# Performance work log

Measured on AMD Instinct MI355X. Metric: run time of the kernel, lower is better.

Reference implementation:

```python
import jax, jax.numpy as jnp
import numpy as np

N_E = 50000
N_R = 1000
E = 800000
E_HIDDEN = 256
R_HIDDEN = 64
NEG_SLOPE = 0.01  # torch F.leaky_relu default


def segment_softmax(logits, seg, num_segments):
    # numerically stable per-segment softmax over edges
    seg_max = jax.ops.segment_max(logits, seg, num_segments=num_segments)
    seg_max = jnp.where(jnp.isfinite(seg_max), seg_max, 0.0)
    ex = jnp.exp(logits - seg_max[seg])
    denom = jax.ops.segment_sum(ex, seg, num_segments=num_segments)
    return ex / (denom[seg] + 1e-16)


def setup_inputs() -> dict:
    key = jax.random.key(0)
    ks = jax.random.split(key, 9)
    return {
        "x_e": jax.random.normal(ks[0], (N_E, E_HIDDEN), dtype=jnp.float32),
        "x_r": jax.random.normal(ks[1], (N_R, R_HIDDEN), dtype=jnp.float32),
        "edge_index": jax.random.randint(ks[2], (2, E), 0, N_E, dtype=jnp.int64),
        "rel": jax.random.randint(ks[3], (E,), 0, N_R, dtype=jnp.int64),
        "line_graph_index": jax.random.randint(ks[4], (2, E), 0, E, dtype=jnp.int64),
        "line_graph_val": jax.random.uniform(ks[5], (E,), dtype=jnp.float32),
        "a_h_w": jax.random.normal(ks[6], (E_HIDDEN,), dtype=jnp.float32),
        "a_t_w": jax.random.normal(ks[7], (E_HIDDEN,), dtype=jnp.float32),
        "a_r_w": jax.random.normal(ks[8], (R_HIDDEN,), dtype=jnp.float32),
    }


def reference(x_e, x_r, edge_index, rel, line_graph_index, line_graph_val, a_h_w, a_t_w, a_r_w):
    head, tail = edge_index[0], edge_index[1]
    # per-node scalar scores, gathered per edge
    s_e_h = jnp.einsum("nd,d->n", x_e, a_h_w)  # [N_e]
    s_e_t = jnp.einsum("nd,d->n", x_e, a_t_w)  # [N_e]
    s_r = jnp.einsum("rd,d->r", x_r, a_r_w)    # [N_r]
    e_h = s_e_h[head]
    e_t = s_e_t[tail]
    e_r = s_r[rel]

    n_e = x_e.shape[0]
    msg = x_r[rel]  # [E, r_hidden]

    # head branch: segment softmax over head groups, scatter-aggregate x_r[rel]
    alpha_h = segment_softmax(jax.nn.leaky_relu(e_h + e_r, NEG_SLOPE), head, n_e)
    x_e_h = jax.ops.segment_sum(alpha_h[:, None] * msg, head, num_segments=n_e)

    # tail branch: softmax grouped by tail, but spmm still scatters into head rows
    alpha_t = segment_softmax(jax.nn.leaky_relu(e_t + e_r, NEG_SLOPE), tail, n_e)
    x_e_t = jax.ops.segment_sum(alpha_t[:, None] * msg, tail, num_segments=n_e)

    return jnp.concatenate([x_e_h, x_e_t], axis=1)  # [N_e, 2*r_hidden]
```

## Files before the change

### kernel.cpp

```cpp
#include <hip/hip_runtime.h>

static constexpr int kNE = 50000;
static constexpr int kNR = 1000;
static constexpr int kE  = 800000;
static constexpr int kEH = 256;
static constexpr int kRH = 64;
static constexpr float kNeg = 0.01f;

static constexpr int kSegsPerB = 64;
static constexpr int kSegs = 2 * kNE;
static constexpr int kB = (kSegs + kSegsPerB - 1) / kSegsPerB;
static constexpr int kCap = 1536;
static constexpr int kEdgesPerBin = 2048;
static constexpr int kChunkRecs  = 2 * kEdgesPerBin;
static constexpr int kBinBlocks  = (kE + kEdgesPerBin - 1) / kEdgesPerBin;
static constexpr int kTabW       = kB + 1;
static constexpr int kNodeBlocks = kNE / 8;
static constexpr int kRelBlocks  = kNR / 8;
static constexpr int kCntPad = 2048;

__device__ __forceinline__ float lrelu(float x){ return x > 0.f ? x : kNeg * x; }

__global__ __launch_bounds__(512) void k_bin_scores(
        const float* __restrict__ xe, const float* __restrict__ ahw,
        const float* __restrict__ atw, const float* __restrict__ xr,
        const float* __restrict__ arw,
        const int* __restrict__ head, const int* __restrict__ tail,
        const int* __restrict__ rel,
        float* __restrict__ s_h, float* __restrict__ s_t, float* __restrict__ s_r,
        unsigned short* __restrict__ chunk, unsigned short* __restrict__ tab){
    __shared__ int cnt[kCntPad];
    __shared__ int cur[kCntPad];
    __shared__ unsigned int srt[kChunkRecs];
    __shared__ int wsum[8];

    int blk = blockIdx.x;
    int tid = threadIdx.x;
    int lane = tid & 63;

    if (blk >= kBinBlocks){
        int sb = blk - kBinBlocks;
        if (sb < kNodeBlocks){
            int node = sb * 8 + (tid >> 6);
            const float4* row = (const float4*)(xe + (size_t)node * kEH);
            float4 xv = row[lane];
            float4 av = ((const float4*)ahw)[lane];
            float4 bv = ((const float4*)atw)[lane];
            float ph = xv.x*av.x + xv.y*av.y + xv.z*av.z + xv.w*av.w;
            float pt = xv.x*bv.x + xv.y*bv.y + xv.z*bv.z + xv.w*bv.w;
            #pragma unroll
            for (int o = 32; o > 0; o >>= 1){
                ph += __shfl_down(ph, o, 64);
                pt += __shfl_down(pt, o, 64);
            }
            if (lane == 0){ s_h[node] = ph; s_t[node] = pt; }
        } else {
            int r = (sb - kNodeBlocks) * 8 + (tid >> 6);
            float p = xr[(size_t)r * kRH + lane] * arw[lane];
            #pragma unroll
            for (int o = 32; o > 0; o >>= 1) p += __shfl_down(p, o, 64);
            if (lane == 0) s_r[r] = p;
        }
        return;
    }

    int e0 = blk * kEdgesPerBin;
    for (int i = tid; i < kCntPad; i += 512) cnt[i] = 0;
    __syncthreads();

    unsigned int recs[8];
    unsigned short rnk[8];
    #pragma unroll
    for (int p = 0; p < 4; ++p){
        int e = e0 + p * 512 + tid;
        unsigned int rh = 0xFFFFFFFFu, rt = 0xFFFFFFFFu;
        unsigned short kh = 0, kt = 0;
        if (e < kE){
            int h = head[e], t = tail[e], r = rel[e];
            rh = ((unsigned int)h << 10) | (unsigned int)r;
            rt = ((unsigned int)(kNE + t) << 10) | (unsigned int)r;
            kh = (unsigned short)atomicAdd(&cnt[rh >> 16], 1);
            kt = (unsigned short)atomicAdd(&cnt[rt >> 16], 1);
        }
        recs[p] = rh; recs[4 + p] = rt;
        rnk[p]  = kh; rnk[4 + p]  = kt;
    }
    __syncthreads();

    int c0 = cnt[4 * tid], c1 = cnt[4 * tid + 1], c2 = cnt[4 * tid + 2], c3 = cnt[4 * tid + 3];
    int v = c0 + c1 + c2 + c3;
    int x = v;
    #pragma unroll
    for (int o = 1; o < 64; o <<= 1){
        int y = __shfl_up(x, o, 64);
        if (lane >= o) x += y;
    }
    int wv = tid >> 6;
    if (lane == 63) wsum[wv] = x;
    __syncthreads();
    int wpre = 0, tot = 0;
    #pragma unroll
    for (int w = 0; w < 8; ++w){
        int s = wsum[w];
        if (w < wv) wpre += s;
        tot += s;
    }
    int base = wpre + x - v;
    cur[4 * tid]     = base;
    cur[4 * tid + 1] = base + c0;
    cur[4 * tid + 2] = base + c0 + c1;
    cur[4 * tid + 3] = base + c0 + c1 + c2;
    __syncthreads();

    #pragma unroll
    for (int p = 0; p < 8; ++p){
        unsigned int rc = recs[p];
        if (rc != 0xFFFFFFFFu){
            int slot = cur[rc >> 16] + (int)rnk[p];
            srt[slot] = rc;
        }
    }
    __syncthreads();

    unsigned int* cw = (unsigned int*)(chunk + (size_t)blk * kChunkRecs);
    for (int j2 = tid; j2 < (tot >> 1); j2 += 512){
        unsigned int lo = srt[2 * j2] & 0xFFFFu;
        unsigned int hi = srt[2 * j2 + 1] & 0xFFFFu;
        cw[j2] = lo | (hi << 16);
    }
    unsigned short* trow = tab + (size_t)blk * kTabW;
    for (int i = tid; i < kB; i += 512) trow[i] = (unsigned short)cur[i];
    if (tid == 0) trow[kB] = (unsigned short)tot;
}

__global__ __launch_bounds__(256) void k_sort_aggregate(
        const unsigned short* __restrict__ chunk, const unsigned short* __restrict__ tab,
        const float* __restrict__ s_h, const float* __restrict__ s_t,
        const float* __restrict__ s_r, const float* __restrict__ xr,
        float* __restrict__ out){
    __shared__ float srl[kNR];
    __shared__ float sn[kSegsPerB];
    __shared__ unsigned short relbuf[kCap];
    __shared__ float alphabuf[kCap];
    __shared__ int cumOff[kBinBlocks + 1];
    __shared__ int srcBase[kBinBlocks];
    __shared__ int cnt[kSegsPerB], start[kSegsPerB];
    __shared__ unsigned int mx[kSegsPerB];
    __shared__ unsigned short order[kSegsPerB];
    __shared__ int gsum[4];

    int b = blockIdx.x;
    int tid = threadIdx.x;
    int lane = tid & 63;
    int wv = tid >> 6;

    for (int i = tid; i < kNR; i += 256) srl[i] = s_r[i];
    if (tid < kSegsPerB){
        cnt[tid] = 0;
        mx[tid] = 0u;
        int gseg = b * kSegsPerB + tid;
        float s = 0.f;
        if (gseg < kNE) s = s_h[gseg];
        else if (gseg < kSegs) s = s_t[gseg - kNE];
        sn[tid] = s;
    }
    if (tid == 0) cumOff[0] = 0;
    __syncthreads();

    int nrecBase = 0;
    for (int c0 = 0; c0 < kBinBlocks; c0 += 256){
        int c = c0 + tid;
        int L = 0;
        if (c < kBinBlocks){
            const unsigned short* trow = tab + (size_t)c * kTabW;
            int s = trow[b];
            L = (int)trow[b + 1] - s;
            srcBase[c] = c * kChunkRecs + s;
        }
        int x = L;
        #pragma unroll
        for (int o = 1; o < 64; o <<= 1){
            int y = __shfl_up(x, o, 64);
            if (lane >= o) x += y;
        }
        if (lane == 63) gsum[wv] = x;
        __syncthreads();
        int wpre = 0, stot = 0;
        #pragma unroll
        for (int w = 0; w < 4; ++w){
            int g = gsum[w];
            if (w < wv) wpre += g;
            stot += g;
        }
        if (c < kBinBlocks) cumOff[c + 1] = nrecBase + wpre + x;
        nrecBase += stot;
        __syncthreads();
    }
    int nrec = nrecBase > kCap ? kCap : nrecBase;

    unsigned short recs[6], rnk[6];
    #pragma unroll
    for (int p = 0; p < 6; ++p){
        int j = p * 256 + tid;
        unsigned short rc = 0xFFFFu, rk = 0;
        if (j < nrec){
            int lo = 0, hi = kBinBlocks;
            #pragma unroll 1
            while (hi - lo > 1){
                int mid = (lo + hi) >> 1;
                if (cumOff[mid] <= j) lo = mid; else hi = mid;
            }
            rc = chunk[srcBase[lo] + (j - cumOff[lo])];
            rk = (unsigned short)atomicAdd(&cnt[rc >> 10], 1);
        }
        recs[p] = rc; rnk[p] = rk;
    }
    __syncthreads();
    if (tid < kSegsPerB){
        int c = cnt[tid];
        int x = c;
        #pragma unroll
        for (int o = 1; o < 64; o <<= 1){
            int y = __shfl_up(x, o, 64);
            if (tid >= o) x += y;
        }
        start[tid] = x - c;

        unsigned int key = ((unsigned int)c << 6) | (unsigned int)tid;
        #pragma unroll
        for (int k = 2; k <= 64; k <<= 1){
            #pragma unroll
            for (int j = k >> 1; j > 0; j >>= 1){
                unsigned int o2 = __shfl_xor(key, j, 64);
                bool keepMin = (((tid & j) == 0) == ((tid & k) == 0));
                unsigned int mn = key < o2 ? key : o2;
                unsigned int mxk = key < o2 ? o2 : key;
                key = keepMin ? mn : mxk;
            }
        }
        order[tid] = (unsigned short)(key & 63u);
    }
    __syncthreads();
    #pragma unroll
    for (int p = 0; p < 6; ++p){
        unsigned short rc = recs[p];
        if (rc != 0xFFFFu){
            int ls = rc >> 10;
            int rr = rc & 1023;
            int slot = start[ls] + (int)rnk[p];
            float lg = lrelu(sn[ls] + srl[rr]);
            unsigned int s32 = __float_as_uint(lg);
            unsigned int key = (s32 & 0x80000000u) ? ~s32 : (s32 | 0x80000000u);
            atomicMax(&mx[ls], key);
            relbuf[slot] = (unsigned short)rr;
            alphabuf[slot] = lg;
        }
    }
    __syncthreads();

    int grp = tid >> 4;
    int sub = tid & 15;
    #pragma unroll
    for (int i = 0; i < 4; ++i){
        int ls = order[i * 16 + grp];
        int gseg = b * kSegsPerB + ls;
        if (gseg >= kSegs) continue;
        int deg = cnt[ls], st = start[ls];

        unsigned int u = mx[ls];
        float m = __uint_as_float((u & 0x80000000u) ? (u & 0x7FFFFFFFu) : ~u);

        float ss = 0.f;
        for (int k = sub; k < deg; k += 16){
            float e = __expf(alphabuf[st + k] - m);
            alphabuf[st + k] = e;
            ss += e;
        }
        #pragma unroll
        for (int o = 1; o < 16; o <<= 1) ss += __shfl_xor(ss, o, 64);
        float inv = 1.f / (ss + 1e-16f);

        float4 acc = {0.f, 0.f, 0.f, 0.f};
        int k = 0;
        for (; k + 4 <= deg; k += 4){
            int r0 = relbuf[st + k],     r1 = relbuf[st + k + 1];
            int r2 = relbuf[st + k + 2], r3 = relbuf[st + k + 3];
            float a0 = alphabuf[st + k],     a1 = alphabuf[st + k + 1];
            float a2 = alphabuf[st + k + 2], a3 = alphabuf[st + k + 3];
            float4 v0 = ((const float4*)(xr + (size_t)r0 * kRH))[sub];
            float4 v1 = ((const float4*)(xr + (size_t)r1 * kRH))[sub];
            float4 v2 = ((const float4*)(xr + (size_t)r2 * kRH))[sub];
            float4 v3 = ((const float4*)(xr + (size_t)r3 * kRH))[sub];
            acc.x += a0*v0.x + a1*v1.x + a2*v2.x + a3*v3.x;
            acc.y += a0*v0.y + a1*v1.y + a2*v2.y + a3*v3.y;
            acc.z += a0*v0.z + a1*v1.z + a2*v2.z + a3*v3.z;
            acc.w += a0*v0.w + a1*v1.w + a2*v2.w + a3*v3.w;
        }
        for (; k < deg; ++k){
            int rr = relbuf[st + k];
            float a = alphabuf[st + k];
            float4 v = ((const float4*)(xr + (size_t)rr * kRH))[sub];
            acc.x += a*v.x; acc.y += a*v.y; acc.z += a*v.z; acc.w += a*v.w;
        }
        acc.x *= inv; acc.y *= inv; acc.z *= inv; acc.w *= inv;

        bool isHead = gseg < kNE;
        int node = isHead ? gseg : gseg - kNE;
        float4* op = (float4*)(out + (size_t)node * (2 * kRH) + (isHead ? 0 : kRH));
        op[sub] = acc;
    }
}

extern "C" void kernel_launch(void* const* d_in, const int* in_sizes, int n_in,
                              void* d_out, int out_size, void* d_ws, size_t ws_size,
                              hipStream_t stream) {
    const float* xe  = (const float*)d_in[0];
    const float* xr  = (const float*)d_in[1];
    const int* edge_index = (const int*)d_in[2];
    const int* rel        = (const int*)d_in[3];
    const float* ahw = (const float*)d_in[6];
    const float* atw = (const float*)d_in[7];
    const float* arw = (const float*)d_in[8];
    float* out = (float*)d_out;

    const int* head = edge_index;
    const int* tail = edge_index + kE;

    char* ws = (char*)d_ws;
    float* s_h  = (float*)ws;                    ws += kNE * sizeof(float);
    float* s_t  = (float*)ws;                    ws += kNE * sizeof(float);
    float* s_r  = (float*)ws;                    ws += ((kNR + 256) & ~255) * sizeof(float);
    unsigned short* chunk = (unsigned short*)ws; ws += (size_t)kBinBlocks * kChunkRecs * sizeof(unsigned short);
    unsigned short* tab   = (unsigned short*)ws; ws += (size_t)kBinBlocks * kTabW * sizeof(unsigned short);

    k_bin_scores<<<kBinBlocks + kNodeBlocks + kRelBlocks, 512, 0, stream>>>(
        xe, ahw, atw, xr, arw, head, tail, rel, s_h, s_t, s_r, chunk, tab);
    k_sort_aggregate<<<kB, 256, 0, stream>>>(chunk, tab, s_h, s_t, s_r, xr, out);
}
```

Measured before the change: 145.5 us.

## Precompute per-bucket chunk offsets in a separate kernel and double edges per bin

```diff
diff --git a/kernel.cpp b/kernel.cpp
--- a/kernel.cpp
+++ b/kernel.cpp
@@ -11,10 +11,12 @@
 static constexpr int kSegs = 2 * kNE;
 static constexpr int kB = (kSegs + kSegsPerB - 1) / kSegsPerB;
 static constexpr int kCap = 1536;
-static constexpr int kEdgesPerBin = 2048;
+static constexpr int kEdgesPerBin = 4096;
 static constexpr int kChunkRecs  = 2 * kEdgesPerBin;
 static constexpr int kBinBlocks  = (kE + kEdgesPerBin - 1) / kEdgesPerBin;
+static constexpr int kChunks     = kBinBlocks;
 static constexpr int kTabW       = kB + 1;
+static constexpr int kTabC       = 208;
 static constexpr int kNodeBlocks = kNE / 8;
 static constexpr int kRelBlocks  = kNR / 8;
 static constexpr int kCntPad = 2048;
@@ -30,9 +32,8 @@
         float* __restrict__ s_h, float* __restrict__ s_t, float* __restrict__ s_r,
         unsigned short* __restrict__ chunk, unsigned short* __restrict__ tab){
     __shared__ int cnt[kCntPad];
-    __shared__ int cur[kCntPad];
     __shared__ unsigned int srt[kChunkRecs];
-    __shared__ int wsum[8];
+    int* wsum = (int*)srt;
 
     int blk = blockIdx.x;
     int tid = threadIdx.x;
@@ -68,10 +69,10 @@
     for (int i = tid; i < kCntPad; i += 512) cnt[i] = 0;
     __syncthreads();
 
-    unsigned int recs[8];
-    unsigned short rnk[8];
-    #pragma unroll
-    for (int p = 0; p < 4; ++p){
+    unsigned int recs[16];
+    unsigned short rnk[16];
+    #pragma unroll
+    for (int p = 0; p < 8; ++p){
         int e = e0 + p * 512 + tid;
         unsigned int rh = 0xFFFFFFFFu, rt = 0xFFFFFFFFu;
         unsigned short kh = 0, kt = 0;
@@ -82,8 +83,8 @@
             kh = (unsigned short)atomicAdd(&cnt[rh >> 16], 1);
             kt = (unsigned short)atomicAdd(&cnt[rt >> 16], 1);
         }
-        recs[p] = rh; recs[4 + p] = rt;
-        rnk[p]  = kh; rnk[4 + p]  = kt;
+        recs[p] = rh; recs[8 + p] = rt;
+        rnk[p]  = kh; rnk[8 + p]  = kt;
     }
     __syncthreads();
 
@@ -106,17 +107,17 @@
         tot += s;
     }
     int base = wpre + x - v;
-    cur[4 * tid]     = base;
-    cur[4 * tid + 1] = base + c0;
-    cur[4 * tid + 2] = base + c0 + c1;
-    cur[4 * tid + 3] = base + c0 + c1 + c2;
-    __syncthreads();
-
-    #pragma unroll
-    for (int p = 0; p < 8; ++p){
+    cnt[4 * tid]     = base;
+    cnt[4 * tid + 1] = base + c0;
+    cnt[4 * tid + 2] = base + c0 + c1;
+    cnt[4 * tid + 3] = base + c0 + c1 + c2;
+    __syncthreads();
+
+    #pragma unroll
+    for (int p = 0; p < 16; ++p){
         unsigned int rc = recs[p];
         if (rc != 0xFFFFFFFFu){
-            int slot = cur[rc >> 16] + (int)rnk[p];
+            int slot = cnt[rc >> 16] + (int)rnk[p];
             srt[slot] = rc;
         }
     }
@@ -129,12 +130,44 @@
         cw[j2] = lo | (hi << 16);
     }
     unsigned short* trow = tab + (size_t)blk * kTabW;
-    for (int i = tid; i < kB; i += 512) trow[i] = (unsigned short)cur[i];
+    for (int i = tid; i < kB; i += 512) trow[i] = (unsigned short)cnt[i];
     if (tid == 0) trow[kB] = (unsigned short)tot;
 }
 
+__global__ __launch_bounds__(256) void k_bucket_tab(
+        const unsigned short* __restrict__ tab,
+        int* __restrict__ cumG, int* __restrict__ srcG){
+    int b = blockIdx.x * 4 + (threadIdx.x >> 6);
+    int lane = threadIdx.x & 63;
+    if (b >= kB) return;
+    int carry = 0;
+    #pragma unroll
+    for (int i = 0; i < (kChunks + 63) / 64; ++i){
+        int c = i * 64 + lane;
+        int s = 0, L = 0;
+        if (c < kChunks){
+            const unsigned short* trow = tab + (size_t)c * kTabW;
+            s = trow[b];
+            L = (int)trow[b + 1] - s;
+        }
+        int x = L;
+        #pragma unroll
+        for (int o = 1; o < 64; o <<= 1){
+            int y = __shfl_up(x, o, 64);
+            if (lane >= o) x += y;
+        }
+        if (c < kChunks){
+            cumG[(size_t)b * kTabC + c] = carry + x - L;
+            srcG[(size_t)b * kTabC + c] = c * kChunkRecs + s;
+        }
+        carry += __shfl(x, 63, 64);
+    }
+    if (lane == 0) cumG[(size_t)b * kTabC + kChunks] = carry;
+}
+
 __global__ __launch_bounds__(256) void k_sort_aggregate(
-        const unsigned short* __restrict__ chunk, const unsigned short* __restrict__ tab,
+        const unsigned short* __restrict__ chunk,
+        const int* __restrict__ cumG, const int* __restrict__ srcG,
         const float* __restrict__ s_h, const float* __restrict__ s_t,
         const float* __restrict__ s_r, const float* __restrict__ xr,
         float* __restrict__ out){
@@ -142,17 +175,14 @@
     __shared__ float sn[kSegsPerB];
     __shared__ unsigned short relbuf[kCap];
     __shared__ float alphabuf[kCap];
-    __shared__ int cumOff[kBinBlocks + 1];
-    __shared__ int srcBase[kBinBlocks];
+    __shared__ int cumOff[kChunks + 1];
+    __shared__ int srcB[kChunks];
     __shared__ int cnt[kSegsPerB], start[kSegsPerB];
     __shared__ unsigned int mx[kSegsPerB];
     __shared__ unsigned short order[kSegsPerB];
-    __shared__ int gsum[4];
 
     int b = blockIdx.x;
     int tid = threadIdx.x;
-    int lane = tid & 63;
-    int wv = tid >> 6;
 
     for (int i = tid; i < kNR; i += 256) srl[i] = s_r[i];
     if (tid < kSegsPerB){
@@ -164,39 +194,16 @@
         else if (gseg < kSegs) s = s_t[gseg - kNE];
         sn[tid] = s;
     }
-    if (tid == 0) cumOff[0] = 0;
-    __syncthreads();
-
-    int nrecBase = 0;
-    for (int c0 = 0; c0 < kBinBlocks; c0 += 256){
-        int c = c0 + tid;
-        int L = 0;
-        if (c < kBinBlocks){
-            const unsigned short* trow = tab + (size_t)c * kTabW;
-            int s = trow[b];
-            L = (int)trow[b + 1] - s;
-            srcBase[c] = c * kChunkRecs + s;
-        }
-        int x = L;
-        #pragma unroll
-        for (int o = 1; o < 64; o <<= 1){
-            int y = __shfl_up(x, o, 64);
-            if (lane >= o) x += y;
-        }
-        if (lane == 63) gsum[wv] = x;
-        __syncthreads();
-        int wpre = 0, stot = 0;
-        #pragma unroll
-        for (int w = 0; w < 4; ++w){
-            int g = gsum[w];
-            if (w < wv) wpre += g;
-            stot += g;
-        }
-        if (c < kBinBlocks) cumOff[c + 1] = nrecBase + wpre + x;
-        nrecBase += stot;
-        __syncthreads();
-    }
-    int nrec = nrecBase > kCap ? kCap : nrecBase;
+    {
+        const int* co = cumG + (size_t)b * kTabC;
+        const int* sg = srcG + (size_t)b * kTabC;
+        if (tid <= kChunks) cumOff[tid] = co[tid];
+        if (tid <  kChunks) srcB[tid]  = sg[tid];
+    }
+    __syncthreads();
+
+    int nrec = cumOff[kChunks];
+    if (nrec > kCap) nrec = kCap;
 
     unsigned short recs[6], rnk[6];
     #pragma unroll
@@ -204,13 +211,13 @@
         int j = p * 256 + tid;
         unsigned short rc = 0xFFFFu, rk = 0;
         if (j < nrec){
-            int lo = 0, hi = kBinBlocks;
+            int lo = 0, hi = kChunks;
             #pragma unroll 1
             while (hi - lo > 1){
                 int mid = (lo + hi) >> 1;
                 if (cumOff[mid] <= j) lo = mid; else hi = mid;
             }
-            rc = chunk[srcBase[lo] + (j - cumOff[lo])];
+            rc = chunk[srcB[lo] + (j - cumOff[lo])];
             rk = (unsigned short)atomicAdd(&cnt[rc >> 10], 1);
         }
         recs[p] = rc; rnk[p] = rk;
@@ -331,9 +338,12 @@
     float* s_t  = (float*)ws;                    ws += kNE * sizeof(float);
     float* s_r  = (float*)ws;                    ws += ((kNR + 256) & ~255) * sizeof(float);
     unsigned short* chunk = (unsigned short*)ws; ws += (size_t)kBinBlocks * kChunkRecs * sizeof(unsigned short);
-    unsigned short* tab   = (unsigned short*)ws; ws += (size_t)kBinBlocks * kTabW * sizeof(unsigned short);
+    unsigned short* tab   = (unsigned short*)ws; ws += ((size_t)kBinBlocks * kTabW * sizeof(unsigned short) + 255) & ~(size_t)255;
+    int* cumG = (int*)ws;                        ws += (size_t)kB * kTabC * sizeof(int);
+    int* srcG = (int*)ws;                        ws += (size_t)kB * kTabC * sizeof(int);
 
     k_bin_scores<<<kBinBlocks + kNodeBlocks + kRelBlocks, 512, 0, stream>>>(
         xe, ahw, atw, xr, arw, head, tail, rel, s_h, s_t, s_r, chunk, tab);
-    k_sort_aggregate<<<kB, 256, 0, stream>>>(chunk, tab, s_h, s_t, s_r, xr, out);
+    k_bucket_tab<<<(kB + 3) / 4, 256, 0, stream>>>(tab, cumG, srcG);
+    k_sort_aggregate<<<kB, 256, 0, stream>>>(chunk, cumG, srcG, s_h, s_t, s_r, xr, out);
 }
```

Measured after the change: 148.5 us. +2.1%, slower.
